# Performance work log

Hardware: AMD Instinct MI355X
Metric: run time of the kernel (lower is better)

The kernel has to match this reference:

```python
import jax, jax.numpy as jnp
import numpy as np

X_DIM, Y_DIM, HIDDEN, N = 768, 768, 300, 768


def setup_inputs() -> dict:
    key = jax.random.key(0)
    ks = jax.random.split(key, 7)
    lim1 = 1.0 / np.sqrt(X_DIM + Y_DIM)
    lim2 = 1.0 / np.sqrt(HIDDEN)
    return {
        "x_samples": jax.random.normal(ks[0], (N, X_DIM), dtype=jnp.float32),
        "y_samples": jax.random.normal(ks[1], (N, Y_DIM), dtype=jnp.float32),
        "perm": jax.random.permutation(ks[2], N).astype(jnp.int32),
        # Linear 1: (x_dim+y_dim) -> hidden, torch default uniform init
        "W1": jax.random.uniform(ks[3], (HIDDEN, X_DIM + Y_DIM), jnp.float32, -lim1, lim1),
        "b1": jax.random.uniform(ks[4], (HIDDEN,), jnp.float32, -lim1, lim1),
        # Linear 2: hidden -> 1
        "W2": jax.random.uniform(ks[5], (1, HIDDEN), jnp.float32, -lim2, lim2),
        "b2": jax.random.uniform(ks[6], (1,), jnp.float32, -lim2, lim2),
    }


def reference(x_samples, y_samples, perm, W1, b1, W2, b2):
    n = x_samples.shape[0]
    x_dim = x_samples.shape[1]
    # First linear is separable across the concat: split W1 into x- and y-parts.
    hx = x_samples @ W1[:, :x_dim].T            # [N, H]
    hy = y_samples @ W1[:, x_dim:].T            # [N, H]
    w2 = W2[0]                                   # [H]
    # T0: matched pairs (x_i, y_i)
    t0 = jax.nn.softplus(jax.nn.relu(hx + hy + b1) @ w2 + b2[0])   # [N]
    # T1[i, j] = F(x_j, y_perm[i]) -- pairwise tile, [N, N, H] intermediate
    hyp = hy[perm]                               # [N, H]
    hpair = jax.nn.relu(hyp[:, None, :] + hx[None, :, :] + b1)     # [N, N, H]
    t1 = jax.nn.softplus(hpair @ w2 + b2[0])     # [N, N]
    lower_bound = t0.mean() - (jax.nn.logsumexp(t1, axis=1).mean() - jnp.log(n).astype(t1.dtype))
    return lower_bound
```

## Files before the change

kernel.cpp:

```cpp
#include <hip/hip_runtime.h>
#include <math.h>

#define NN   768
#define HH   300
#define LDH  320
#define KD   768

#define P_OFF   0
#define P_STR   245760
#define CF_OFF  3932160
#define AF_OFF  4177920
#define SP_OFF  4423680
#define SP_STR  589824
#define ES_OFF  9142272
#define T0_OFF  9143040

__global__ __launch_bounds__(256) void k1_gemm(
    const float* __restrict__ x, const float* __restrict__ y,
    const int* __restrict__ perm, const float* __restrict__ W1,
    float* __restrict__ wsf)
{
    const int tid = threadIdx.x;
    const int tx = tid & 15;
    const int ty = tid >> 4;
    const int i0 = blockIdx.x * 128;
    const int h0 = blockIdx.y * 64;
    const int gemm = blockIdx.z & 1;
    const int ks   = blockIdx.z >> 1;
    const int kbeg = ks * 96;

    const float* src = gemm ? y : x;
    const int koff = gemm ? KD : 0;

    __shared__ float xs[32][132];
    __shared__ float ws[32][68];

    float4 acc[8];
    #pragma unroll
    for (int r = 0; r < 8; ++r) acc[r] = make_float4(0.f,0.f,0.f,0.f);

    for (int kc = 0; kc < 96; kc += 32) {
        const int kb = kbeg + kc;
        #pragma unroll
        for (int it = 0; it < 4; ++it) {
            int e = tid + it * 256;
            int row = e >> 3, kq = (e & 7) << 2;
            int grow = i0 + row;
            if (gemm) grow = perm[grow];
            float4 v = *(const float4*)(src + (size_t)grow * KD + kb + kq);
            xs[kq+0][row] = v.x; xs[kq+1][row] = v.y;
            xs[kq+2][row] = v.z; xs[kq+3][row] = v.w;
        }
        #pragma unroll
        for (int it = 0; it < 2; ++it) {
            int e = tid + it * 256;
            int hrow = e >> 3, kq = (e & 7) << 2;
            int hg = h0 + hrow;
            float4 v = make_float4(0.f,0.f,0.f,0.f);
            if (hg < HH) v = *(const float4*)(W1 + (size_t)hg * (2*KD) + koff + kb + kq);
            ws[kq+0][hrow] = v.x; ws[kq+1][hrow] = v.y;
            ws[kq+2][hrow] = v.z; ws[kq+3][hrow] = v.w;
        }
        __syncthreads();

        #pragma unroll 8
        for (int k = 0; k < 32; ++k) {
            float4 a0 = *(const float4*)&xs[k][4*ty];
            float4 a1 = *(const float4*)&xs[k][64 + 4*ty];
            float4 b  = *(const float4*)&ws[k][4*tx];
            acc[0].x = fmaf(a0.x,b.x,acc[0].x); acc[0].y = fmaf(a0.x,b.y,acc[0].y);
            acc[0].z = fmaf(a0.x,b.z,acc[0].z); acc[0].w = fmaf(a0.x,b.w,acc[0].w);
            acc[1].x = fmaf(a0.y,b.x,acc[1].x); acc[1].y = fmaf(a0.y,b.y,acc[1].y);
            acc[1].z = fmaf(a0.y,b.z,acc[1].z); acc[1].w = fmaf(a0.y,b.w,acc[1].w);
            acc[2].x = fmaf(a0.z,b.x,acc[2].x); acc[2].y = fmaf(a0.z,b.y,acc[2].y);
            acc[2].z = fmaf(a0.z,b.z,acc[2].z); acc[2].w = fmaf(a0.z,b.w,acc[2].w);
            acc[3].x = fmaf(a0.w,b.x,acc[3].x); acc[3].y = fmaf(a0.w,b.y,acc[3].y);
            acc[3].z = fmaf(a0.w,b.z,acc[3].z); acc[3].w = fmaf(a0.w,b.w,acc[3].w);
            acc[4].x = fmaf(a1.x,b.x,acc[4].x); acc[4].y = fmaf(a1.x,b.y,acc[4].y);
            acc[4].z = fmaf(a1.x,b.z,acc[4].z); acc[4].w = fmaf(a1.x,b.w,acc[4].w);
            acc[5].x = fmaf(a1.y,b.x,acc[5].x); acc[5].y = fmaf(a1.y,b.y,acc[5].y);
            acc[5].z = fmaf(a1.y,b.z,acc[5].z); acc[5].w = fmaf(a1.y,b.w,acc[5].w);
            acc[6].x = fmaf(a1.z,b.x,acc[6].x); acc[6].y = fmaf(a1.z,b.y,acc[6].y);
            acc[6].z = fmaf(a1.z,b.z,acc[6].z); acc[6].w = fmaf(a1.z,b.w,acc[6].w);
            acc[7].x = fmaf(a1.w,b.x,acc[7].x); acc[7].y = fmaf(a1.w,b.y,acc[7].y);
            acc[7].z = fmaf(a1.w,b.z,acc[7].z); acc[7].w = fmaf(a1.w,b.w,acc[7].w);
        }
        __syncthreads();
    }

    float* dst = wsf + P_OFF + (size_t)(gemm*8 + ks) * P_STR;
    #pragma unroll
    for (int r = 0; r < 8; ++r) {
        int i = i0 + ((r < 4) ? (4*ty + r) : (64 + 4*ty + r - 4));
        *(float4*)(dst + (size_t)i * LDH + h0 + 4*tx) = acc[r];
    }
}

__global__ __launch_bounds__(256) void k1b_combine(
    const float* __restrict__ b1, float* __restrict__ wsf)
{
    const int HQ = LDH/4;
    const int PER = NN * HQ;
    int idx = blockIdx.x * 256 + threadIdx.x;
    int gemm = idx >= PER ? 1 : 0;
    int rem = idx - gemm * PER;
    int i = rem / HQ;
    int h4 = (rem % HQ) * 4;

    float4 out = make_float4(0.f,0.f,0.f,0.f);
    if (h4 < HH) {
        const float* p = wsf + P_OFF + (size_t)gemm*8*P_STR + (size_t)i*LDH + h4;
        #pragma unroll
        for (int ks = 0; ks < 8; ++ks) {
            float4 v = *(const float4*)(p + (size_t)ks * P_STR);
            out.x += v.x; out.y += v.y; out.z += v.z; out.w += v.w;
        }
        if (gemm) {
            float4 bv = *(const float4*)(b1 + h4);
            out.x += bv.x; out.y += bv.y; out.z += bv.z; out.w += bv.w;
        }
    }
    float* dst = wsf + (gemm ? AF_OFF : CF_OFF);
    *(float4*)(dst + (size_t)i * LDH + h4) = out;
}

__global__ __launch_bounds__(256) void k2_pair(
    const float* __restrict__ wsf, const float* __restrict__ w2,
    float* __restrict__ sp)
{
    const int tid = threadIdx.x;
    const int tx = tid & 15;
    const int ty = tid >> 4;
    const int i0 = blockIdx.x * 64;
    const int j0 = blockIdx.y * 128;
    const int p  = blockIdx.z;
    const int h0 = p * 40;

    const float* Af = wsf + AF_OFF;
    const float* Cf = wsf + CF_OFF;

    __shared__ float As[40][68];
    __shared__ float Cs[40][132];
    __shared__ float ws2[40];

    for (int e = tid; e < 640; e += 256) {
        int r = e / 10, q = (e % 10) * 4;
        float4 v = *(const float4*)(Af + (size_t)(i0 + r) * LDH + h0 + q);
        As[q+0][r] = v.x; As[q+1][r] = v.y; As[q+2][r] = v.z; As[q+3][r] = v.w;
    }
    for (int e = tid; e < 1280; e += 256) {
        int r = e / 10, q = (e % 10) * 4;
        float4 v = *(const float4*)(Cf + (size_t)(j0 + r) * LDH + h0 + q);
        Cs[q+0][r] = v.x; Cs[q+1][r] = v.y; Cs[q+2][r] = v.z; Cs[q+3][r] = v.w;
    }
    if (tid < 40) {
        int h = h0 + tid;
        ws2[tid] = (h < HH) ? w2[h] : 0.f;
    }
    __syncthreads();

    float4 a0 = make_float4(0,0,0,0);
    float acc[4][8];
    #pragma unroll
    for (int r = 0; r < 4; ++r)
        #pragma unroll
        for (int c = 0; c < 8; ++c) acc[r][c] = 0.f;

    #pragma unroll 4
    for (int h = 0; h < 40; ++h) {
        float wh = ws2[h];
        float4 av = *(const float4*)&As[h][4*ty];
        float4 c0 = *(const float4*)&Cs[h][4*tx];
        float4 c1 = *(const float4*)&Cs[h][64 + 4*tx];
        float ar[4] = {av.x, av.y, av.z, av.w};
        float cr[8] = {c0.x, c0.y, c0.z, c0.w, c1.x, c1.y, c1.z, c1.w};
        #pragma unroll
        for (int r = 0; r < 4; ++r) {
            #pragma unroll
            for (int c = 0; c < 8; ++c) {
                float t = fmaxf(ar[r] + cr[c], 0.f);
                acc[r][c] = fmaf(t, wh, acc[r][c]);
            }
        }
    }

    float* dst = sp + (size_t)p * SP_STR;
    #pragma unroll
    for (int r = 0; r < 4; ++r) {
        int i = i0 + 4*ty + r;
        *(float4*)(dst + (size_t)i * NN + j0 + 4*tx)      =
            make_float4(acc[r][0], acc[r][1], acc[r][2], acc[r][3]);
        *(float4*)(dst + (size_t)i * NN + j0 + 64 + 4*tx) =
            make_float4(acc[r][4], acc[r][5], acc[r][6], acc[r][7]);
    }
}

__global__ __launch_bounds__(256) void k2e_rows(
    const float* __restrict__ wsf, const int* __restrict__ perm,
    const float* __restrict__ w2, const float* __restrict__ b2,
    float* __restrict__ esum, float* __restrict__ t0out)
{
    const int tid = threadIdx.x;
    __shared__ float red[256];
    const float b2v = b2[0];

    if ((int)blockIdx.x < NN) {
        const int row = blockIdx.x;
        const float* spr = wsf + SP_OFF + (size_t)row * NN;
        float e = 0.f;
        #pragma unroll
        for (int jj = 0; jj < 3; ++jj) {
            int j = tid + jj * 256;
            float s = 0.f;
            #pragma unroll
            for (int p = 0; p < 8; ++p) s += spr[(size_t)p * SP_STR + j];
            e += expf(s + b2v);
        }
        red[tid] = e;
        __syncthreads();
        for (int s = 128; s > 0; s >>= 1) {
            if (tid < s) red[tid] += red[tid + s];
            __syncthreads();
        }
        if (tid == 0) esum[row] = red[0];
    } else {
        const int row = blockIdx.x - NN;
        const int pr = perm[row];
        const float* Af = wsf + AF_OFF + (size_t)row * LDH;
        const float* Cf = wsf + CF_OFF + (size_t)pr  * LDH;
        float acc = 0.f;
        for (int h = tid; h < HH; h += 256) {
            float z = fmaxf(Af[h] + Cf[h], 0.f);
            acc = fmaf(z, w2[h], acc);
        }
        red[tid] = acc;
        __syncthreads();
        for (int s = 128; s > 0; s >>= 1) {
            if (tid < s) red[tid] += red[tid + s];
            __syncthreads();
        }
        if (tid == 0) {
            float u = red[0] + b2v;
            t0out[row] = (u > 0.f) ? u + log1pf(expf(-u)) : log1pf(expf(u));
        }
    }
}

__global__ __launch_bounds__(256) void k3_final(
    const float* __restrict__ wsf, float* __restrict__ out)
{
    const int tid = threadIdx.x;
    const float* esum = wsf + ES_OFF;
    const float* t0   = wsf + T0_OFF;

    double st0 = 0.0, slse = 0.0;
    for (int i = tid; i < NN; i += 256) {
        st0  += (double)t0[i];
        slse += log((double)NN + (double)esum[i]);
    }
    __shared__ double sa[256], sb[256];
    sa[tid] = st0; sb[tid] = slse;
    __syncthreads();
    for (int s = 128; s > 0; s >>= 1) {
        if (tid < s) { sa[tid] += sa[tid+s]; sb[tid] += sb[tid+s]; }
        __syncthreads();
    }
    if (tid == 0) {
        double lb = sa[0]/(double)NN - (sb[0]/(double)NN - log((double)NN));
        out[0] = (float)lb;
    }
}

extern "C" void kernel_launch(void* const* d_in, const int* in_sizes, int n_in,
                              void* d_out, int out_size, void* d_ws, size_t ws_size,
                              hipStream_t stream) {
    const float* x    = (const float*)d_in[0];
    const float* y    = (const float*)d_in[1];
    const int*   perm = (const int*)  d_in[2];
    const float* W1   = (const float*)d_in[3];
    const float* b1   = (const float*)d_in[4];
    const float* W2   = (const float*)d_in[5];
    const float* b2   = (const float*)d_in[6];
    float* wsf = (float*)d_ws;
    float* out = (float*)d_out;

    k1_gemm    <<<dim3(6,5,16), 256, 0, stream>>>(x, y, perm, W1, wsf);
    k1b_combine<<<480,          256, 0, stream>>>(b1, wsf);
    k2_pair    <<<dim3(12,6,8), 256, 0, stream>>>(wsf, W2, wsf + SP_OFF);
    k2e_rows   <<<2*NN,         256, 0, stream>>>(wsf, perm, W2, b2,
                                                  wsf + ES_OFF, wsf + T0_OFF);
    k3_final   <<<1,            256, 0, stream>>>(wsf, out);
}
```

Baseline: 126.5 us.

## Drop split-K GMEM combine, transpose hidden layout, retile pair kernel

The first GEMM drops split-K and now accumulates the full K range per block, adding the bias in its epilogue. This removes the separate combine kernel and the large partial-sum buffer. Hidden activations are stored as [H][N], so the pair kernel can load tiles with plain float4 copies instead of transposing in shared memory, and it splits H into 4 chunks of 75 rather than 8 of 40. That halves the partial-score traffic to the row-reduction kernel, and the t0 path becomes one thread per column. The cost is fewer blocks in the GEMM (240 versus 480) with a long serial K loop and small per-thread tiles, and a smaller per-thread tile (6x3) in the pair kernel.

```diff
diff --git a/kernel.cpp b/kernel.cpp
--- a/kernel.cpp
+++ b/kernel.cpp
@@ -3,125 +3,81 @@
 
 #define NN   768
 #define HH   300
-#define LDH  320
+#define HPAD 320
 #define KD   768
 
-#define P_OFF   0
-#define P_STR   245760
-#define CF_OFF  3932160
-#define AF_OFF  4177920
-#define SP_OFF  4423680
+#define CF_OFF  0
+#define AF_OFF  245760
+#define SP_OFF  491520
 #define SP_STR  589824
-#define ES_OFF  9142272
-#define T0_OFF  9143040
+#define ES_OFF  2850816
+#define T0_OFF  2851584
 
 __global__ __launch_bounds__(256) void k1_gemm(
     const float* __restrict__ x, const float* __restrict__ y,
     const int* __restrict__ perm, const float* __restrict__ W1,
-    float* __restrict__ wsf)
+    const float* __restrict__ b1, float* __restrict__ wsf)
 {
     const int tid = threadIdx.x;
     const int tx = tid & 15;
     const int ty = tid >> 4;
-    const int i0 = blockIdx.x * 128;
-    const int h0 = blockIdx.y * 64;
-    const int gemm = blockIdx.z & 1;
-    const int ks   = blockIdx.z >> 1;
-    const int kbeg = ks * 96;
-
-    const float* src = gemm ? y : x;
-    const int koff = gemm ? KD : 0;
-
-    __shared__ float xs[32][132];
-    __shared__ float ws[32][68];
-
-    float4 acc[8];
-    #pragma unroll
-    for (int r = 0; r < 8; ++r) acc[r] = make_float4(0.f,0.f,0.f,0.f);
-
-    for (int kc = 0; kc < 96; kc += 32) {
-        const int kb = kbeg + kc;
-        #pragma unroll
-        for (int it = 0; it < 4; ++it) {
-            int e = tid + it * 256;
-            int row = e >> 3, kq = (e & 7) << 2;
-            int grow = i0 + row;
-            if (gemm) grow = perm[grow];
-            float4 v = *(const float4*)(src + (size_t)grow * KD + kb + kq);
-            xs[kq+0][row] = v.x; xs[kq+1][row] = v.y;
-            xs[kq+2][row] = v.z; xs[kq+3][row] = v.w;
-        }
-        #pragma unroll
-        for (int it = 0; it < 2; ++it) {
-            int e = tid + it * 256;
-            int hrow = e >> 3, kq = (e & 7) << 2;
-            int hg = h0 + hrow;
-            float4 v = make_float4(0.f,0.f,0.f,0.f);
-            if (hg < HH) v = *(const float4*)(W1 + (size_t)hg * (2*KD) + koff + kb + kq);
-            ws[kq+0][hrow] = v.x; ws[kq+1][hrow] = v.y;
-            ws[kq+2][hrow] = v.z; ws[kq+3][hrow] = v.w;
-        }
+    const int i0 = blockIdx.x * 64;
+    const int h0 = blockIdx.y * 32;
+    const int g  = blockIdx.z;
+
+    const float* src = g ? y : x;
+
+    __shared__ float Xt[32][66];
+    __shared__ float Wt[32][34];
+
+    float4 acc0 = make_float4(0.f,0.f,0.f,0.f);
+    float4 acc1 = make_float4(0.f,0.f,0.f,0.f);
+
+    const int kq = (tid & 7) << 2;
+    int r0 = i0 + (tid >> 3);
+    int r1 = r0 + 32;
+    if (g) { r0 = perm[r0]; r1 = perm[r1]; }
+    const float* xp0 = src + (size_t)r0 * KD + kq;
+    const float* xp1 = src + (size_t)r1 * KD + kq;
+    const int wrow = tid >> 3;
+    const int hg = h0 + wrow;
+    const float* wp = W1 + (size_t)hg * (2*KD) + (g ? KD : 0) + kq;
+    const bool hvalid = hg < HH;
+
+    for (int kb = 0; kb < KD; kb += 32) {
+        float4 v0 = *(const float4*)(xp0 + kb);
+        float4 v1 = *(const float4*)(xp1 + kb);
+        float4 w  = make_float4(0.f,0.f,0.f,0.f);
+        if (hvalid) w = *(const float4*)(wp + kb);
+        __syncthreads();
+        Xt[kq+0][tid>>3]      = v0.x; Xt[kq+1][tid>>3]      = v0.y;
+        Xt[kq+2][tid>>3]      = v0.z; Xt[kq+3][tid>>3]      = v0.w;
+        Xt[kq+0][32+(tid>>3)] = v1.x; Xt[kq+1][32+(tid>>3)] = v1.y;
+        Xt[kq+2][32+(tid>>3)] = v1.z; Xt[kq+3][32+(tid>>3)] = v1.w;
+        Wt[kq+0][wrow] = w.x; Wt[kq+1][wrow] = w.y;
+        Wt[kq+2][wrow] = w.z; Wt[kq+3][wrow] = w.w;
         __syncthreads();
 
         #pragma unroll 8
         for (int k = 0; k < 32; ++k) {
-            float4 a0 = *(const float4*)&xs[k][4*ty];
-            float4 a1 = *(const float4*)&xs[k][64 + 4*ty];
-            float4 b  = *(const float4*)&ws[k][4*tx];
-            acc[0].x = fmaf(a0.x,b.x,acc[0].x); acc[0].y = fmaf(a0.x,b.y,acc[0].y);
-            acc[0].z = fmaf(a0.x,b.z,acc[0].z); acc[0].w = fmaf(a0.x,b.w,acc[0].w);
-            acc[1].x = fmaf(a0.y,b.x,acc[1].x); acc[1].y = fmaf(a0.y,b.y,acc[1].y);
-            acc[1].z = fmaf(a0.y,b.z,acc[1].z); acc[1].w = fmaf(a0.y,b.w,acc[1].w);
-            acc[2].x = fmaf(a0.z,b.x,acc[2].x); acc[2].y = fmaf(a0.z,b.y,acc[2].y);
-            acc[2].z = fmaf(a0.z,b.z,acc[2].z); acc[2].w = fmaf(a0.z,b.w,acc[2].w);
-            acc[3].x = fmaf(a0.w,b.x,acc[3].x); acc[3].y = fmaf(a0.w,b.y,acc[3].y);
-            acc[3].z = fmaf(a0.w,b.z,acc[3].z); acc[3].w = fmaf(a0.w,b.w,acc[3].w);
-            acc[4].x = fmaf(a1.x,b.x,acc[4].x); acc[4].y = fmaf(a1.x,b.y,acc[4].y);
-            acc[4].z = fmaf(a1.x,b.z,acc[4].z); acc[4].w = fmaf(a1.x,b.w,acc[4].w);
-            acc[5].x = fmaf(a1.y,b.x,acc[5].x); acc[5].y = fmaf(a1.y,b.y,acc[5].y);
-            acc[5].z = fmaf(a1.y,b.z,acc[5].z); acc[5].w = fmaf(a1.y,b.w,acc[5].w);
-            acc[6].x = fmaf(a1.z,b.x,acc[6].x); acc[6].y = fmaf(a1.z,b.y,acc[6].y);
-            acc[6].z = fmaf(a1.z,b.z,acc[6].z); acc[6].w = fmaf(a1.z,b.w,acc[6].w);
-            acc[7].x = fmaf(a1.w,b.x,acc[7].x); acc[7].y = fmaf(a1.w,b.y,acc[7].y);
-            acc[7].z = fmaf(a1.w,b.z,acc[7].z); acc[7].w = fmaf(a1.w,b.w,acc[7].w);
-        }
-        __syncthreads();
-    }
-
-    float* dst = wsf + P_OFF + (size_t)(gemm*8 + ks) * P_STR;
+            float2 a = *(const float2*)&Wt[k][2*ty];
+            float4 b = *(const float4*)&Xt[k][4*tx];
+            acc0.x = fmaf(a.x,b.x,acc0.x); acc0.y = fmaf(a.x,b.y,acc0.y);
+            acc0.z = fmaf(a.x,b.z,acc0.z); acc0.w = fmaf(a.x,b.w,acc0.w);
+            acc1.x = fmaf(a.y,b.x,acc1.x); acc1.y = fmaf(a.y,b.y,acc1.y);
+            acc1.z = fmaf(a.y,b.z,acc1.z); acc1.w = fmaf(a.y,b.w,acc1.w);
+        }
+    }
+
+    float* dstBase = wsf + (g ? AF_OFF : CF_OFF);
     #pragma unroll
-    for (int r = 0; r < 8; ++r) {
-        int i = i0 + ((r < 4) ? (4*ty + r) : (64 + 4*ty + r - 4));
-        *(float4*)(dst + (size_t)i * LDH + h0 + 4*tx) = acc[r];
-    }
-}
-
-__global__ __launch_bounds__(256) void k1b_combine(
-    const float* __restrict__ b1, float* __restrict__ wsf)
-{
-    const int HQ = LDH/4;
-    const int PER = NN * HQ;
-    int idx = blockIdx.x * 256 + threadIdx.x;
-    int gemm = idx >= PER ? 1 : 0;
-    int rem = idx - gemm * PER;
-    int i = rem / HQ;
-    int h4 = (rem % HQ) * 4;
-
-    float4 out = make_float4(0.f,0.f,0.f,0.f);
-    if (h4 < HH) {
-        const float* p = wsf + P_OFF + (size_t)gemm*8*P_STR + (size_t)i*LDH + h4;
-        #pragma unroll
-        for (int ks = 0; ks < 8; ++ks) {
-            float4 v = *(const float4*)(p + (size_t)ks * P_STR);
-            out.x += v.x; out.y += v.y; out.z += v.z; out.w += v.w;
-        }
-        if (gemm) {
-            float4 bv = *(const float4*)(b1 + h4);
-            out.x += bv.x; out.y += bv.y; out.z += bv.z; out.w += bv.w;
-        }
-    }
-    float* dst = wsf + (gemm ? AF_OFF : CF_OFF);
-    *(float4*)(dst + (size_t)i * LDH + h4) = out;
+    for (int r = 0; r < 2; ++r) {
+        int hh = h0 + 2*ty + r;
+        float bias = (g && hh < HH) ? b1[hh] : 0.f;
+        float4 o = (r == 0) ? acc0 : acc1;
+        o.x += bias; o.y += bias; o.z += bias; o.w += bias;
+        *(float4*)(dstBase + (size_t)hh * NN + i0 + 4*tx) = o;
+    }
 }
 
 __global__ __launch_bounds__(256) void k2_pair(
@@ -131,53 +87,50 @@
     const int tid = threadIdx.x;
     const int tx = tid & 15;
     const int ty = tid >> 4;
-    const int i0 = blockIdx.x * 64;
-    const int j0 = blockIdx.y * 128;
+    const int j0 = blockIdx.x * 48;
+    const int i0 = blockIdx.y * 96;
     const int p  = blockIdx.z;
-    const int h0 = p * 40;
-
-    const float* Af = wsf + AF_OFF;
-    const float* Cf = wsf + CF_OFF;
-
-    __shared__ float As[40][68];
-    __shared__ float Cs[40][132];
-    __shared__ float ws2[40];
-
-    for (int e = tid; e < 640; e += 256) {
-        int r = e / 10, q = (e % 10) * 4;
-        float4 v = *(const float4*)(Af + (size_t)(i0 + r) * LDH + h0 + q);
-        As[q+0][r] = v.x; As[q+1][r] = v.y; As[q+2][r] = v.z; As[q+3][r] = v.w;
-    }
-    for (int e = tid; e < 1280; e += 256) {
-        int r = e / 10, q = (e % 10) * 4;
-        float4 v = *(const float4*)(Cf + (size_t)(j0 + r) * LDH + h0 + q);
-        Cs[q+0][r] = v.x; Cs[q+1][r] = v.y; Cs[q+2][r] = v.z; Cs[q+3][r] = v.w;
-    }
-    if (tid < 40) {
-        int h = h0 + tid;
-        ws2[tid] = (h < HH) ? w2[h] : 0.f;
-    }
+    const int h0 = p * 75;
+
+    const float* AF = wsf + AF_OFF;
+    const float* CF = wsf + CF_OFF;
+
+    __shared__ float As[75][100];
+    __shared__ float Cs[75][48];
+    __shared__ float w2s[75];
+
+    for (int e = tid; e < 1800; e += 256) {
+        int h = e / 24, q = (e % 24) * 4;
+        float4 v = *(const float4*)(AF + (size_t)(h0 + h) * NN + i0 + q);
+        *(float4*)&As[h][q] = v;
+    }
+    for (int e = tid; e < 900; e += 256) {
+        int h = e / 12, q = (e % 12) * 4;
+        float4 v = *(const float4*)(CF + (size_t)(h0 + h) * NN + j0 + q);
+        *(float4*)&Cs[h][q] = v;
+    }
+    if (tid < 75) w2s[tid] = w2[h0 + tid];
     __syncthreads();
 
-    float4 a0 = make_float4(0,0,0,0);
-    float acc[4][8];
+    float acc[6][3];
     #pragma unroll
-    for (int r = 0; r < 4; ++r)
+    for (int r = 0; r < 6; ++r)
         #pragma unroll
-        for (int c = 0; c < 8; ++c) acc[r][c] = 0.f;
-
-    #pragma unroll 4
-    for (int h = 0; h < 40; ++h) {
-        float wh = ws2[h];
-        float4 av = *(const float4*)&As[h][4*ty];
-        float4 c0 = *(const float4*)&Cs[h][4*tx];
-        float4 c1 = *(const float4*)&Cs[h][64 + 4*tx];
-        float ar[4] = {av.x, av.y, av.z, av.w};
-        float cr[8] = {c0.x, c0.y, c0.z, c0.w, c1.x, c1.y, c1.z, c1.w};
+        for (int c = 0; c < 3; ++c) acc[r][c] = 0.f;
+
+    #pragma unroll 5
+    for (int h = 0; h < 75; ++h) {
+        float wh = w2s[h];
+        float4 a0 = *(const float4*)&As[h][4*ty];
+        float2 a1 = *(const float2*)&As[h][64 + 2*ty];
+        float2 c0 = *(const float2*)&Cs[h][2*tx];
+        float  c2 = Cs[h][32 + tx];
+        float ar[6] = {a0.x, a0.y, a0.z, a0.w, a1.x, a1.y};
+        float cr[3] = {c0.x, c0.y, c2};
         #pragma unroll
-        for (int r = 0; r < 4; ++r) {
+        for (int r = 0; r < 6; ++r) {
             #pragma unroll
-            for (int c = 0; c < 8; ++c) {
+            for (int c = 0; c < 3; ++c) {
                 float t = fmaxf(ar[r] + cr[c], 0.f);
                 acc[r][c] = fmaf(t, wh, acc[r][c]);
             }
@@ -186,12 +139,11 @@
 
     float* dst = sp + (size_t)p * SP_STR;
     #pragma unroll
-    for (int r = 0; r < 4; ++r) {
-        int i = i0 + 4*ty + r;
-        *(float4*)(dst + (size_t)i * NN + j0 + 4*tx)      =
-            make_float4(acc[r][0], acc[r][1], acc[r][2], acc[r][3]);
-        *(float4*)(dst + (size_t)i * NN + j0 + 64 + 4*tx) =
-            make_float4(acc[r][4], acc[r][5], acc[r][6], acc[r][7]);
+    for (int r = 0; r < 6; ++r) {
+        int i = i0 + ((r < 4) ? (4*ty + r) : (64 + 2*ty + (r - 4)));
+        float* rp = dst + (size_t)i * NN + j0;
+        *(float2*)(rp + 2*tx) = make_float2(acc[r][0], acc[r][1]);
+        rp[32 + tx] = acc[r][2];
     }
 }
 
@@ -201,19 +153,20 @@
     float* __restrict__ esum, float* __restrict__ t0out)
 {
     const int tid = threadIdx.x;
-    __shared__ float red[256];
     const float b2v = b2[0];
 
     if ((int)blockIdx.x < NN) {
+        __shared__ float red[256];
         const int row = blockIdx.x;
         const float* spr = wsf + SP_OFF + (size_t)row * NN;
         float e = 0.f;
         #pragma unroll
         for (int jj = 0; jj < 3; ++jj) {
             int j = tid + jj * 256;
-            float s = 0.f;
-            #pragma unroll
-            for (int p = 0; p < 8; ++p) s += spr[(size_t)p * SP_STR + j];
+            float s = spr[j];
+            s += spr[(size_t)1 * SP_STR + j];
+            s += spr[(size_t)2 * SP_STR + j];
+            s += spr[(size_t)3 * SP_STR + j];
             e += expf(s + b2v);
         }
         red[tid] = e;
@@ -224,25 +177,19 @@
         }
         if (tid == 0) esum[row] = red[0];
     } else {
-        const int row = blockIdx.x - NN;
-        const int pr = perm[row];
-        const float* Af = wsf + AF_OFF + (size_t)row * LDH;
-        const float* Cf = wsf + CF_OFF + (size_t)pr  * LDH;
-        float acc = 0.f;
-        for (int h = tid; h < HH; h += 256) {
-            float z = fmaxf(Af[h] + Cf[h], 0.f);
-            acc = fmaf(z, w2[h], acc);
-        }
-        red[tid] = acc;
-        __syncthreads();
-        for (int s = 128; s > 0; s >>= 1) {
-            if (tid < s) red[tid] += red[tid + s];
-            __syncthreads();
-        }
-        if (tid == 0) {
-            float u = red[0] + b2v;
-            t0out[row] = (u > 0.f) ? u + log1pf(expf(-u)) : log1pf(expf(u));
-        }
+        const int col = ((int)blockIdx.x - NN) * 256 + tid;
+        const int pcol = perm[col];
+        const float* AF = wsf + AF_OFF;
+        const float* CF = wsf + CF_OFF;
+        float s = 0.f;
+        for (int h = 0; h < HH; ++h) {
+            float a = AF[(size_t)h * NN + col];
+            float c = CF[(size_t)h * NN + pcol];
+            float z = fmaxf(a + c, 0.f);
+            s = fmaf(z, w2[h], s);
+        }
+        float u = s + b2v;
+        t0out[col] = (u > 0.f) ? u + log1pf(expf(-u)) : log1pf(expf(u));
     }
 }
 
@@ -284,10 +231,9 @@
     float* wsf = (float*)d_ws;
     float* out = (float*)d_out;
 
-    k1_gemm    <<<dim3(6,5,16), 256, 0, stream>>>(x, y, perm, W1, wsf);
-    k1b_combine<<<480,          256, 0, stream>>>(b1, wsf);
-    k2_pair    <<<dim3(12,6,8), 256, 0, stream>>>(wsf, W2, wsf + SP_OFF);
-    k2e_rows   <<<2*NN,         256, 0, stream>>>(wsf, perm, W2, b2,
-                                                  wsf + ES_OFF, wsf + T0_OFF);
-    k3_final   <<<1,            256, 0, stream>>>(wsf, out);
-}
+    k1_gemm  <<<dim3(12,10,2), 256, 0, stream>>>(x, y, perm, W1, b1, wsf);
+    k2_pair  <<<dim3(16,8,4),  256, 0, stream>>>(wsf, W2, wsf + SP_OFF);
+    k2e_rows <<<NN + 3,        256, 0, stream>>>(wsf, perm, W2, b2,
+                                                 wsf + ES_OFF, wsf + T0_OFF);
+    k3_final <<<1,             256, 0, stream>>>(wsf, out);
+}
```

Result: slower. 152.5 us (+20.6%).
